# Kernel tuning notes

Measured on AMD Instinct MI355X. Metric: run time of the kernel, lower is better.

Reference implementation:

```python
import jax, jax.numpy as jnp
import numpy as np

N, E = 3000, 48000
FEAT, HID, OUT = 32, 32, 8
R, K, N_CONV = 2, 5, 2
RATIO = 0.9  # TopKPooling ratio


def _glorot(key, o, i):
    return jax.random.normal(key, (o, i), jnp.float32) * (1.0 / np.sqrt(i))


def setup_inputs() -> dict:
    key = jax.random.key(0)
    ks = jax.random.split(key, 13)
    x = jax.random.normal(ks[0], (N, FEAT), jnp.float32)
    row = jax.random.randint(ks[1], (E,), 0, N, dtype=jnp.int32)
    col = jax.random.randint(ks[2], (E,), 0, N, dtype=jnp.int32)
    col = jnp.where(col == row, (col + 1) % N, col)  # no self loops
    edge_index = jnp.stack([row, col])
    return {
        "x": x,
        "edge_index": edge_index,
        "h": jnp.float32(0.5),       # learnable zoom parameter
        "alpha": jnp.float32(0.1),   # learnable spectral shift
        "Wr0": _glorot(ks[3], HID, FEAT),
        "Wc0a": _glorot(ks[4], HID, FEAT),  # Re(ComplexLinear.weight); Im part never reaches the output
        "Wc0b": _glorot(ks[5], HID, FEAT),
        "Wr1": _glorot(ks[6], HID, HID),
        "Wc1a": _glorot(ks[7], HID, HID),
        "Wc1b": _glorot(ks[8], HID, HID),
        "pool_w": jax.random.normal(ks[9], (HID,), jnp.float32),
        "lin_weight": _glorot(ks[10], OUT, HID),
        "lin_bias": jax.random.normal(ks[11], (OUT,), jnp.float32) * 0.01,
    }


def _cayley_conv(x, edge_index, h, alpha, Wr, Wcs):
    # Dense Jacobi iteration approximating the Cayley spectral filter.
    # The original builds 2n x 2n block matrices [[T,0],[0,B]] whose off-
    # diagonal blocks are zero and whose bottom-half state starts at (and
    # provably stays) zero, so we compute the identical top block only and
    # append the zero bottom half at the end (matching the (2n, C) output).
    n = x.shape[0]
    row, col = edge_index[0], edge_index[1]
    deg = jnp.zeros((n,), x.dtype).at[row].add(1.0)            # scatter-add degree
    A = jnp.zeros((n, n), x.dtype).at[row, col].set(1.0)       # dense adjacency (set, like L[row,col]=w)
    idx = jnp.arange(n)
    dvals = deg - alpha                                        # shifted Laplacian diagonal
    L = (-A).at[idx, idx].set(dvals)                           # L = D - A - alpha*I, dense
    Off = L.at[idx, idx].set(0.0)                              # off-diagonal part (NOT scaled by h)
    invD = 1.0 / (dvals * h)                                   # inverse of diag(h*L)
    b_mat = invD[:, None] * (h * L)                            # extended_tmp_Dia @ extended_tmp_right (top block)
    J = -(Off * invD[None, :])                                 # jacobi = -Off @ D^{-1} (top block)
    out = x @ Wr.T                                             # real_linear([x;0]) top half
    y = x
    for Wc in Wcs:                                             # r polynomial orders
        b_j = b_mat @ y
        yk = b_j
        for _ in range(K):                                     # K Jacobi iterations
            yk = J @ yk + b_j
        y = yk
        out = out + 2.0 * (y @ Wc.T)                           # 2*Re(ComplexLinear(y)), y real => only Re(W) contributes
    return jnp.concatenate([out, jnp.zeros_like(out)], axis=0)  # (2n, C_out)


def reference(x, edge_index, h, alpha, Wr0, Wc0a, Wc0b, Wr1, Wc1a, Wc1b, pool_w, lin_weight, lin_bias):
    x1 = jax.nn.relu(_cayley_conv(x, edge_index, h, alpha, Wr0, [Wc0a, Wc0b]))
    x2 = jax.nn.relu(_cayley_conv(x1, edge_index, h, alpha, Wr1, [Wc1a, Wc1b]))
    n_total = x2.shape[0]                      # 4N: each conv doubles node count
    k = int(np.ceil(RATIO * n_total))          # TopKPooling(ratio=0.9), static k
    score = jnp.tanh((x2 @ pool_w) / jnp.linalg.norm(pool_w))
    vals, perm = jax.lax.top_k(score, k)
    xp = x2[perm] * vals[:, None]              # gate selected nodes by tanh-score
    g = jnp.mean(xp, axis=0)                   # global_mean_pool (single graph)
    # dropout(p=0.2) is identity in eval mode
    return (g @ lin_weight.T + lin_bias)[None, :]  # (1, OUT)
```

## Files before the change

### kernel.cpp

```cpp
#include <hip/hip_runtime.h>
#include <hip/hip_bf16.h>

typedef __hip_bfloat16 bf16;
typedef unsigned short u16;
typedef unsigned int   u32;

#define NN 3000
#define EE 48000
#define NF 32
#define KEXC 1200
#define KDEN 10800.0f
#define NB 32
#define NT 1024
#define CT 1024
#define SEG 94
#define CS  47
#define SLOTS 48128
#define DUMMYC 3070u
#define PADROW 3071u
#define FLUSHB 0x40000000u

#define OFF_CNT  0u
#define OFF_TOT  128u
#define OFF_EXC  256u
#define OFF_SLOT 512u
#define OFF_WINV 193024u
#define OFF_XT   205056u
#define OFF_Y1   589056u
#define OFF_Y2   973056u
#define OFF_X1T  1357056u
#define OFF_X2T  1741056u

__device__ __forceinline__ bool scalar_is_bf16(const void* hp) {
    return ((const unsigned short*)hp)[0] != 0x0000;
}
__device__ __forceinline__ bool tensor_is_bf16(const void* xp) {
    const unsigned short* u = (const unsigned short*)xp;
    int cnt = 0;
    for (int k = 0; k < 16; k++) {
        unsigned e = (u[2 * k] >> 7) & 0xFF;
        if (e >= 107 && e <= 147) cnt++;
    }
    return cnt >= 12;
}
__device__ __forceinline__ float ldv(const void* p, int i, bool b16) {
    return b16 ? __bfloat162float(((const bf16*)p)[i]) : ((const float*)p)[i];
}

__global__ void __launch_bounds__(NT)
k_csr(const int* __restrict__ ei, const void* __restrict__ x,
      const void* hp, const void* ap,
      float* __restrict__ winv, u32* __restrict__ slotT,
      float* __restrict__ xT, u32* __restrict__ zhdr) {
    __shared__ u16 tmp_c[4096], tmp_r[4096], stage[4096], rid[4096];
    __shared__ int s_deg[128], sA[128];
    __shared__ int lcur[96];
    __shared__ int s_base, s_cnt;
    __shared__ int s_fl[2];
    const int t = threadIdx.x, blk = blockIdx.x;

    if (t == 0) {
        s_fl[0] = scalar_is_bf16(hp) ? 1 : 0;
        s_fl[1] = tensor_is_bf16(x) ? 1 : 0;
        s_base = 0; s_cnt = 0;
    }
    if (blk == 0 && t < 96) zhdr[t] = 0u;
    if (t < 128) s_deg[t] = 0;
    if (t < 96) lcur[t] = 0;
    __syncthreads();
    const bool sbf = s_fl[0] != 0, xtb = s_fl[1] != 0;
    const float hh = ldv(hp, 0, sbf), aa = ldv(ap, 0, sbf);

    const int r0 = blk * SEG;
    const int r1 = (r0 + SEG < NN) ? (r0 + SEG) : NN;

    for (int idx = t; idx < SEG * NF; idx += NT) {
        int f = idx / SEG, ii = idx % SEG;
        int i = r0 + ii;
        if (i < NN) xT[f * NN + i] = ldv(x, i * NF + f, xtb);
    }

    const int4* ei4 = (const int4*)ei;
    const int lane = t & 63;
    const unsigned long long below = (lane == 63) ? ~0ull >> 1
                                   : ((1ull << lane) - 1ull);
    int cntlt = 0;
    for (int e4 = t; e4 < EE / 4; e4 += NT) {
        int4 rv = ei4[e4];
        int rr[4] = { rv.x, rv.y, rv.z, rv.w };
#pragma unroll
        for (int k = 0; k < 4; k++) {
            int r = rr[k];
            bool own = (r >= r0 && r < r1);
            unsigned long long mask = __ballot(own);
            if (mask) {
                int leader = (int)__ffsll((long long)mask) - 1;
                int wbase = 0;
                if (lane == leader)
                    wbase = atomicAdd(&s_cnt, (int)__popcll(mask));
                wbase = __shfl(wbase, leader);
                if (own) {
                    int p = wbase + (int)__popcll(mask & below);
                    tmp_c[p] = (u16)ei[EE + e4 * 4 + k];
                    tmp_r[p] = (u16)(r - r0);
                    atomicAdd(&s_deg[r - r0], 1);
                }
            }
            cntlt += (r < r0) ? 1 : 0;
        }
    }
#pragma unroll
    for (int o = 32; o > 0; o >>= 1) cntlt += __shfl_down(cntlt, o);
    if ((t & 63) == 0 && cntlt) atomicAdd(&s_base, cntlt);
    __syncthreads();
    const int base = s_base;
    const int cnt  = s_cnt;

    if (t < r1 - r0)
        winv[r0 + t] = 1.0f / (hh * ((float)s_deg[t] - aa));

    if (t < 96) sA[t] = s_deg[t];
    __syncthreads();
#pragma unroll
    for (int d = 1; d < 96; d <<= 1) {
        int v = 0;
        if (t < 96) v = sA[t] + ((t >= d) ? sA[t - d] : 0);
        __syncthreads();
        if (t < 96) sA[t] = v;
        __syncthreads();
    }
#define LPEX(rr) ((rr) == 0 ? 0 : sA[(rr) - 1])

    for (int l = t; l < cnt; l += NT) {
        int rr = tmp_r[l];
        int pos = atomicAdd(&lcur[rr], 1);
        stage[LPEX(rr) + pos] = tmp_c[l];
    }
    __syncthreads();
    for (int rr = t; rr < (r1 - r0); rr += NT) {
        int s0 = LPEX(rr), s1 = LPEX(rr + 1);
        for (int s2 = s0; s2 < s1; s2++) rid[s2] = (u16)rr;
    }
    __syncthreads();
    for (int ls = t; ls < cnt; ls += NT) {
        int rr = rid[ls];
        int rs = LPEX(rr);
        u16 c = stage[ls];
        bool dup = false;
        for (int ls2 = rs; ls2 < ls; ls2++) dup |= (stage[ls2] == c);
        if (dup) stage[ls] = (u16)DUMMYC;
    }
    __syncthreads();
    for (int ls = t; ls < cnt; ls += NT) {
        int rr = rid[ls];
        int s = base + ls;
        int rs = base + LPEX(rr), re = base + LPEX(rr + 1);
        int tc = s / CS, j = s % CS;
        bool atEnd = (s == re - 1), atRange = (j == CS - 1);
        bool flush = atEnd || atRange;
        int frag = tc - rs / CS; if (frag > 3) frag = 3;
        u32 pidx = ((u32)(r0 + rr) << 2) | (u32)frag;
        u32 p = (u32)stage[ls] | (pidx << 12)
              | (flush ? FLUSHB : 0u);
        slotT[j * CT + tc] = p;
    }
    if (blk == 31) {
        for (int s = EE + t; s < SLOTS; s += NT) {
            int tc = s / CS, j = s % CS;
            slotT[j * CT + tc] = DUMMYC | ((PADROW << 2) << 12)
                               | ((j == CS - 1) ? FLUSHB : 0u);
        }
    }
#undef LPEX
}

__global__ void __launch_bounds__(CT, 1)
k_chains(const float* __restrict__ xinT, const void* hp,
         const u32* __restrict__ slotT, const float* __restrict__ winv,
         float* __restrict__ y1g, float* __restrict__ y2g) {
    __shared__ float s_y[3072], s_sys[3072], s_b[3072], s_w[3072];
    __shared__ float s_part[3072 * 4];
    __shared__ int s_fl[1];
    const int t = threadIdx.x, blk = blockIdx.x;

    if (t == 0) s_fl[0] = scalar_is_bf16(hp) ? 1 : 0;
    __syncthreads();
    const float hh = ldv(hp, 0, s_fl[0] != 0);

    u32 sl[CS];
#pragma unroll
    for (int j = 0; j < CS; j++) sl[j] = slotT[j * CT + t];

#pragma unroll
    for (int k = 0; k < 3; k++) {
        int i = t + k * CT;
        float v = (i < NN) ? xinT[blk * NN + i] : 0.0f;
        float w = (i < NN) ? winv[i] : 0.0f;
        s_w[i] = w; s_y[i] = v; s_sys[i] = w * v;
    }
    for (int i = t; i < 3072 * 4; i += CT) s_part[i] = 0.0f;
    __syncthreads();

#pragma unroll 1
    for (int ord = 0; ord < 2; ord++) {
#pragma unroll 1
        for (int step = 0; step < 6; step++) {
            const float* src = (step == 0) ? s_y : s_sys;
            float acc = 0.f;
#pragma unroll
            for (int s = 0; s < CS; s++) {
                u32 p = sl[s];
                acc += src[p & 0xFFFu];
                if (p & FLUSHB) {
                    s_part[(p >> 12) & 0x3FFFu] = acc;
                    acc = 0.f;
                }
            }
            __syncthreads();
            if (step == 0) {
#pragma unroll
                for (int k = 0; k < 3; k++) {
                    int i = t + k * CT;
                    const float4 pr = *(const float4*)&s_part[i * 4];
                    float a = (pr.x + pr.y) + (pr.z + pr.w);
                    float nb = s_y[i] - hh * s_w[i] * a;
                    s_b[i] = nb; s_y[i] = nb; s_sys[i] = s_w[i] * nb;
                }
            } else {
#pragma unroll
                for (int k = 0; k < 3; k++) {
                    int i = t + k * CT;
                    const float4 pr = *(const float4*)&s_part[i * 4];
                    float a = (pr.x + pr.y) + (pr.z + pr.w);
                    float y = s_b[i] + a;
                    s_y[i] = y; s_sys[i] = s_w[i] * y;
                }
            }
            __syncthreads();
        }
        float* yg = (ord == 0) ? y1g : y2g;
#pragma unroll
        for (int k = 0; k < 3; k++) {
            int i = t + k * CT;
            if (i < NN) yg[blk * NN + i] = s_y[i];
        }
    }
}

__global__ void __launch_bounds__(256)
k_gemmT(const float* __restrict__ xinT,
        const void* __restrict__ Wr, const void* __restrict__ Wa, const void* __restrict__ Wb,
        const float* __restrict__ y1T, const float* __restrict__ y2T,
        float* __restrict__ outT) {
    __shared__ float sW[96];
    __shared__ int s_fl;
    const int t = threadIdx.x, o = blockIdx.y;
    if (t == 0) s_fl = tensor_is_bf16(Wr) ? 1 : 0;
    __syncthreads();
    const bool wtb = s_fl != 0;
    if (t < 96) {
        sW[t] = (t < 32) ? ldv(Wr, o * 32 + t, wtb)
              : (t < 64) ? 2.0f * ldv(Wa, o * 32 + (t - 32), wtb)
                         : 2.0f * ldv(Wb, o * 32 + (t - 64), wtb);
    }
    __syncthreads();
    int i = blockIdx.x * 256 + t;
    if (i >= NN) return;
    float acc = 0.f;
#pragma unroll
    for (int f = 0; f < NF; f++)
        acc += xinT[f * NN + i] * sW[f]
             + y1T[f * NN + i] * sW[32 + f]
             + y2T[f * NN + i] * sW[64 + f];
    outT[o * NN + i] = fmaxf(acc, 0.f);
}

__global__ void __launch_bounds__(512)
k_pool(const float* __restrict__ x2T, const void* __restrict__ pwp,
       const void* __restrict__ lwp, const void* __restrict__ lbp,
       u32* __restrict__ cntg, float* __restrict__ totf, float* __restrict__ excf,
       void* __restrict__ outp) {
    __shared__ float s_s[3072];
    __shared__ float red[512];
    __shared__ int rnk[96];
    __shared__ int s_fl, s_last;
    const int t = threadIdx.x, blk = blockIdx.x;
    const int PNT = 512;

    if (t == 0) s_fl = tensor_is_bf16(pwp) ? 1 : 0;
    __syncthreads();
    const bool tb = s_fl != 0;
    float pw[32];
    float nrm2 = 0.f;
#pragma unroll
    for (int f = 0; f < NF; f++) { pw[f] = ldv(pwp, f, tb); nrm2 += pw[f] * pw[f]; }
    const float nrm = sqrtf(nrm2);

    for (int i = t; i < 3072; i += PNT) {
        if (i < NN) {
            float d = 0.f;
#pragma unroll
            for (int f = 0; f < NF; f++) d += x2T[f * NN + i] * pw[f];
            s_s[i] = tanhf(d / nrm);
        } else s_s[i] = 0.f;
    }
    if (t < 96) rnk[t] = 0;
    __syncthreads();

    const int j0 = blk * SEG;
    const int j1 = (j0 + SEG < NN) ? (j0 + SEG) : NN;
    for (int u = t; u < SEG * 5; u += PNT) {
        int lr = u / 5, i = j0 + lr;
        if (i < j1) {
            float si = s_s[i];
            if (si < 0.f) {
                int seg = (u % 5) * 600;
                int c2 = 0;
                for (int j = seg; j < seg + 600 && j < NN; j++) {
                    float sj = s_s[j];
                    c2 += (sj < si) || ((sj == si) && (j > i));
                }
                if (c2) atomicAdd(&rnk[lr], c2);
            }
        }
    }
    __syncthreads();

    int f = t & 31, rl = t >> 5;
    float at = 0.f, ae = 0.f;
    for (int lr = rl; lr < SEG; lr += 16) {
        int i = j0 + lr;
        if (i < j1) {
            float si = s_s[i];
            float term = x2T[f * NN + i] * si;
            at += term;
            if (si < 0.f && rnk[lr] < KEXC) ae += term;
        }
    }
    red[t] = at; __syncthreads();
    for (int s = 256; s >= 32; s >>= 1) { if (t < s) red[t] += red[t + s]; __syncthreads(); }
    if (t < 32) atomicAdd(&totf[t], red[t]);
    __syncthreads();
    red[t] = ae; __syncthreads();
    for (int s = 256; s >= 32; s >>= 1) { if (t < s) red[t] += red[t + s]; __syncthreads(); }
    if (t < 32) atomicAdd(&excf[t], red[t]);
    __syncthreads();

    if (t == 0) {
        __threadfence();
        u32 old = atomicAdd(cntg, 1u);
        s_last = (old == NB - 1) ? 1 : 0;
    }
    __syncthreads();
    if (s_last) {
        __threadfence();
        if (t < 8) {
            float o = ldv(lbp, t, tb);
            for (int ff = 0; ff < NF; ff++) {
                float tv = __hip_atomic_load(&totf[ff], __ATOMIC_RELAXED, __HIP_MEMORY_SCOPE_AGENT);
                float ev = __hip_atomic_load(&excf[ff], __ATOMIC_RELAXED, __HIP_MEMORY_SCOPE_AGENT);
                o += ((tv - ev) / KDEN) * ldv(lwp, t * 32 + ff, tb);
            }
            if (tb) ((bf16*)outp)[t] = __float2bfloat16(o);
            else    ((float*)outp)[t] = o;
        }
    }
}

extern "C" void kernel_launch(void* const* d_in, const int* in_sizes, int n_in,
                              void* d_out, int out_size, void* d_ws, size_t ws_size,
                              hipStream_t stream) {
    const void* x   = d_in[0];
    const int*  ei  = (const int*)d_in[1];
    const void* hp  = d_in[2];
    const void* ap  = d_in[3];
    const void* Wr0 = d_in[4];
    const void* Wa0 = d_in[5];
    const void* Wb0 = d_in[6];
    const void* Wr1 = d_in[7];
    const void* Wa1 = d_in[8];
    const void* Wb1 = d_in[9];
    const void* pw  = d_in[10];
    const void* lw  = d_in[11];
    const void* lb  = d_in[12];
    char* ws = (char*)d_ws;

    u32*   cntg  = (u32*)(ws + OFF_CNT);
    float* totf  = (float*)(ws + OFF_TOT);
    float* excf  = (float*)(ws + OFF_EXC);
    u32*   slotT = (u32*)(ws + OFF_SLOT);
    float* winv  = (float*)(ws + OFF_WINV);
    float* xT    = (float*)(ws + OFF_XT);
    float* y1g   = (float*)(ws + OFF_Y1);
    float* y2g   = (float*)(ws + OFF_Y2);
    float* x1T   = (float*)(ws + OFF_X1T);
    float* x2T   = (float*)(ws + OFF_X2T);

    k_csr   <<<dim3(32),     dim3(NT),  0, stream>>>(ei, x, hp, ap, winv, slotT, xT, (u32*)ws);
    k_chains<<<dim3(32),     dim3(CT),  0, stream>>>(xT, hp, slotT, winv, y1g, y2g);
    k_gemmT <<<dim3(12, 32), dim3(256), 0, stream>>>(xT, Wr0, Wa0, Wb0, y1g, y2g, x1T);
    k_chains<<<dim3(32),     dim3(CT),  0, stream>>>(x1T, hp, slotT, winv, y1g, y2g);
    k_gemmT <<<dim3(12, 32), dim3(256), 0, stream>>>(x1T, Wr1, Wa1, Wb1, y1g, y2g, x2T);
    k_pool  <<<dim3(32),     dim3(512), 0, stream>>>(x2T, pw, lw, lb, cntg, totf, excf, d_out);
}
```

Before: 252.9 us.

## Reorder CSR column slots per row to reduce LDS bank conflicts in chains

```diff
diff --git a/kernel.cpp b/kernel.cpp
--- a/kernel.cpp
+++ b/kernel.cpp
@@ -52,7 +52,8 @@
       const void* hp, const void* ap,
       float* __restrict__ winv, u32* __restrict__ slotT,
       float* __restrict__ xT, u32* __restrict__ zhdr) {
-    __shared__ u16 tmp_c[4096], tmp_r[4096], stage[4096], rid[4096];
+    __shared__ u16 tmp_c[4096], tmp_r[4096], stage[4096];
+    __shared__ u16 scr[94 * 64];
     __shared__ int s_deg[128], sA[128];
     __shared__ int lcur[96];
     __shared__ int s_base, s_cnt;
@@ -137,32 +138,62 @@
         stage[LPEX(rr) + pos] = tmp_c[l];
     }
     __syncthreads();
-    for (int rr = t; rr < (r1 - r0); rr += NT) {
-        int s0 = LPEX(rr), s1 = LPEX(rr + 1);
-        for (int s2 = s0; s2 < s1; s2++) rid[s2] = (u16)rr;
-    }
-    __syncthreads();
-    for (int ls = t; ls < cnt; ls += NT) {
-        int rr = rid[ls];
-        int rs = LPEX(rr);
-        u16 c = stage[ls];
-        bool dup = false;
-        for (int ls2 = rs; ls2 < ls; ls2++) dup |= (stage[ls2] == c);
-        if (dup) stage[ls] = (u16)DUMMYC;
-    }
-    __syncthreads();
-    for (int ls = t; ls < cnt; ls += NT) {
-        int rr = rid[ls];
-        int s = base + ls;
-        int rs = base + LPEX(rr), re = base + LPEX(rr + 1);
-        int tc = s / CS, j = s % CS;
-        bool atEnd = (s == re - 1), atRange = (j == CS - 1);
-        bool flush = atEnd || atRange;
-        int frag = tc - rs / CS; if (frag > 3) frag = 3;
-        u32 pidx = ((u32)(r0 + rr) << 2) | (u32)frag;
-        u32 p = (u32)stage[ls] | (pidx << 12)
-              | (flush ? FLUSHB : 0u);
-        slotT[j * CT + tc] = p;
+
+    if (t < r1 - r0) {
+        const int rr = t;
+        int rs_l = LPEX(rr), re_l = LPEX(rr + 1);
+        int deg = re_l - rs_l;
+        if (deg > 0) {
+            for (int a = 1; a < deg; a++) {
+                u16 c = stage[rs_l + a];
+                if (c != (u16)DUMMYC) {
+                    for (int b2 = 0; b2 < a; b2++)
+                        if (stage[rs_l + b2] == c) { stage[rs_l + a] = (u16)DUMMYC; break; }
+                }
+            }
+            int rs = base + rs_l, re = base + re_l;
+            int tc0 = rs / CS;
+            u16* my = &scr[rr * 64];
+            for (int tc = tc0; tc <= (re - 1) / CS; tc++) {
+                int c0 = tc * CS;
+                int p0 = (rs > c0) ? rs : c0;
+                int p1 = (re < c0 + CS) ? re : (c0 + CS);
+                int fl = p1 - p0;
+                int f0 = (p0 - rs);
+                unsigned long long usedC = 0ull;
+                for (int q = 0; q < fl; q++) my[q] = 0xFFFFu;
+                for (int q = 0; q < fl; q++) {
+                    int j = (p0 + q) - c0;
+                    int tb = (tc + j) & 31;
+                    for (int c = 0; c < fl; c++) {
+                        if (!((usedC >> c) & 1ull)) {
+                            u16 cv = stage[rs_l + f0 + c];
+                            if (((int)cv & 31) == tb) {
+                                my[q] = cv; usedC |= 1ull << c; break;
+                            }
+                        }
+                    }
+                }
+                {
+                    int c = 0;
+                    for (int q = 0; q < fl; q++) {
+                        if (my[q] == 0xFFFFu) {
+                            while ((usedC >> c) & 1ull) c++;
+                            my[q] = stage[rs_l + f0 + c];
+                            usedC |= 1ull << c;
+                        }
+                    }
+                }
+                int frag = tc - tc0; if (frag > 3) frag = 3;
+                u32 pidx = ((u32)(r0 + rr) << 2) | (u32)frag;
+                for (int q = 0; q < fl; q++) {
+                    int p = p0 + q;
+                    int j = p - c0;
+                    slotT[j * CT + tc] = (u32)my[q] | (pidx << 12)
+                                       | ((p == p1 - 1) ? FLUSHB : 0u);
+                }
+            }
+        }
     }
     if (blk == 31) {
         for (int s = EE + t; s < SLOTS; s += NT) {
```

New measurement: 445.9 us. 1.76x slower.

## Reorder CSR chunk column placement to spread LDS bank accesses in chain kernel

Applied to the files above, without the earlier changes.

```diff
diff --git a/kernel.cpp b/kernel.cpp
--- a/kernel.cpp
+++ b/kernel.cpp
@@ -19,6 +19,8 @@
 #define DUMMYC 3070u
 #define PADROW 3071u
 #define FLUSHB 0x40000000u
+#define NFRAGMAX 160
+#define FSTRIDE 112
 
 #define OFF_CNT  0u
 #define OFF_TOT  128u
@@ -53,16 +55,18 @@
       float* __restrict__ winv, u32* __restrict__ slotT,
       float* __restrict__ xT, u32* __restrict__ zhdr) {
     __shared__ u16 tmp_c[4096], tmp_r[4096], stage[4096], rid[4096];
+    __shared__ u16 fscr[NFRAGMAX * FSTRIDE];
+    __shared__ u32 flist[NFRAGMAX];
     __shared__ int s_deg[128], sA[128];
     __shared__ int lcur[96];
-    __shared__ int s_base, s_cnt;
+    __shared__ int s_base, s_cnt, s_nfrag;
     __shared__ int s_fl[2];
     const int t = threadIdx.x, blk = blockIdx.x;
 
     if (t == 0) {
         s_fl[0] = scalar_is_bf16(hp) ? 1 : 0;
         s_fl[1] = tensor_is_bf16(x) ? 1 : 0;
-        s_base = 0; s_cnt = 0;
+        s_base = 0; s_cnt = 0; s_nfrag = 0;
     }
     if (blk == 0 && t < 96) zhdr[t] = 0u;
     if (t < 128) s_deg[t] = 0;
@@ -141,6 +145,16 @@
         int s0 = LPEX(rr), s1 = LPEX(rr + 1);
         for (int s2 = s0; s2 < s1; s2++) rid[s2] = (u16)rr;
     }
+    if (t < r1 - r0) {
+        int rs_l = LPEX(t), re_l = LPEX(t + 1);
+        if (re_l > rs_l) {
+            int rs = base + rs_l, re = base + re_l;
+            for (int tc = rs / CS; tc <= (re - 1) / CS; tc++) {
+                int pos = atomicAdd(&s_nfrag, 1);
+                flist[pos] = (u32)t | ((u32)tc << 8);
+            }
+        }
+    }
     __syncthreads();
     for (int ls = t; ls < cnt; ls += NT) {
         int rr = rid[ls];
@@ -151,18 +165,49 @@
         if (dup) stage[ls] = (u16)DUMMYC;
     }
     __syncthreads();
-    for (int ls = t; ls < cnt; ls += NT) {
-        int rr = rid[ls];
-        int s = base + ls;
-        int rs = base + LPEX(rr), re = base + LPEX(rr + 1);
-        int tc = s / CS, j = s % CS;
-        bool atEnd = (s == re - 1), atRange = (j == CS - 1);
-        bool flush = atEnd || atRange;
-        int frag = tc - rs / CS; if (frag > 3) frag = 3;
-        u32 pidx = ((u32)(r0 + rr) << 2) | (u32)frag;
-        u32 p = (u32)stage[ls] | (pidx << 12)
-              | (flush ? FLUSHB : 0u);
-        slotT[j * CT + tc] = p;
+    const int nfrag = s_nfrag;
+
+    for (int f = t; f < nfrag; f += NT) {
+        u32 info = flist[f];
+        int rr = (int)(info & 0xFFu);
+        int tc = (int)(info >> 8);
+        int rs_l = LPEX(rr), re_l = LPEX(rr + 1);
+        int rs = base + rs_l, re = base + re_l;
+        int tc0 = rs / CS;
+        int c0 = tc * CS;
+        int p0 = (rs > c0) ? rs : c0;
+        int p1 = (re < c0 + CS) ? re : (c0 + CS);
+        int fl = p1 - p0;
+        int f0 = p0 - rs;
+        u16* srt  = &fscr[f * FSTRIDE];
+        u16* cntb = srt + 48;
+        u16* endb = srt + 80;
+        for (int b = 0; b < 32; b++) cntb[b] = 0;
+        for (int c = 0; c < fl; c++) cntb[stage[rs_l + f0 + c] & 31]++;
+        { int run = 0;
+          for (int b = 0; b < 32; b++) { run += cntb[b]; endb[b] = (u16)run; } }
+        for (int c = 0; c < fl; c++) {
+            u16 cv = stage[rs_l + f0 + c];
+            int b = cv & 31;
+            srt[endb[b] - cntb[b]] = cv;
+            cntb[b]--;
+        }
+        for (int b = 0; b < 32; b++)
+            cntb[b] = endb[b] - (b ? endb[b - 1] : 0);
+        int fragi = tc - tc0; if (fragi > 3) fragi = 3;
+        const u32 pidx = ((u32)(r0 + rr) << 2) | (u32)fragi;
+        int fb = 0;
+        for (int q = 0; q < fl; q++) {
+            int j = (p0 + q) - c0;
+            int tb = (tc + j) & 31;
+            int b;
+            if (cntb[tb] > 0) b = tb;
+            else { while (fb < 31 && cntb[fb] == 0) fb++; b = fb; }
+            u16 cv = srt[endb[b] - cntb[b]];
+            cntb[b]--;
+            slotT[j * CT + tc] = (u32)cv | (pidx << 12)
+                               | ((p0 + q == p1 - 1) ? FLUSHB : 0u);
+        }
     }
     if (blk == 31) {
         for (int s = EE + t; s < SLOTS; s += NT) {
```

After: 285.3 us. 1.13x slower.
